# Performance work log

Hardware: AMD Instinct MI355X
Metric: run time of the kernel (lower is better)

## Reference

```python
import jax, jax.numpy as jnp
import numpy as np

B, S, HID = 1, 2048, 3584
NUM_HEADS, KV_HEADS, HEAD_DIM = 28, 4, 128
MROPE = [16, 24, 24]
HEAVY_RATIO, RECENT_RATIO, SINK, MIN_SEQ = 0.1, 0.1, 4, 1024
SCALING = HEAD_DIM ** -0.5
ROPE_THETA = 1000000.0


def rotate_half(x):
    h = x.shape[-1] // 2
    return jnp.concatenate([-x[..., h:], x[..., :h]], axis=-1)


def apply_mrope(q, k, cos, sin, mrope_section):
    # cos/sin: [3, B, S, head_dim]; interleave sections from the 3 position axes
    sec = mrope_section * 2
    splits = list(np.cumsum(sec)[:-1])
    cos_m = jnp.concatenate([m[i % 3] for i, m in enumerate(jnp.split(cos, splits, axis=-1))], axis=-1)[:, None]  # [B,1,S,D]
    sin_m = jnp.concatenate([m[i % 3] for i, m in enumerate(jnp.split(sin, splits, axis=-1))], axis=-1)[:, None]
    q_emb = q * cos_m + rotate_half(q) * sin_m
    k_emb = k * cos_m + rotate_half(k) * sin_m
    return q_emb, k_emb


def h2o_keep_mask(attn_weights, kv_len):
    # attn_weights: [B, H, Q, KV] post-softmax; accumulated score per head/key
    scores = attn_weights.sum(axis=(0, 2))  # [H, KV]
    heavy = max(1, int(HEAVY_RATIO * kv_len))
    recent = max(1, int(RECENT_RATIO * kv_len))
    keep = jnp.zeros((NUM_HEADS, kv_len), dtype=bool)
    ips = max(SINK * 2, int(0.2 * kv_len))  # image-protect prefix
    if kv_len > 3 * ips:
        keep = keep.at[:, :ips].set(True)
        ms = ips
    else:
        keep = keep.at[:, :SINK].set(True)
        ms = SINK
    keep = keep.at[:, kv_len - recent:].set(True)
    me = kv_len - recent
    k = min(heavy, me - ms)
    _, idx = jax.lax.top_k(scores[:, ms:me], k)  # [H, k]
    keep = keep.at[jnp.arange(NUM_HEADS)[:, None], idx + ms].set(True)
    return keep[None, :, None, :]  # [1, H, 1, KV]


def setup_inputs() -> dict:
    key = jax.random.key(0)
    ks = jax.random.split(key, 8)
    hidden_states = jax.random.normal(ks[0], (B, S, HID), jnp.float32)
    # additive causal mask
    causal = jnp.triu(jnp.full((S, S), -1e9, jnp.float32), k=1)
    attention_mask = causal[None, None]
    # mrope cos/sin (same positions on all 3 axes for text-only prefill)
    inv_freq = 1.0 / (ROPE_THETA ** (jnp.arange(0, HEAD_DIM, 2, dtype=jnp.float32) / HEAD_DIM))
    pos = jnp.arange(S, dtype=jnp.float32)
    freqs = pos[:, None] * inv_freq[None, :]            # [S, D/2]
    emb = jnp.concatenate([freqs, freqs], axis=-1)      # [S, D]
    cos = jnp.broadcast_to(jnp.cos(emb)[None, None], (3, B, S, HEAD_DIM))
    sin = jnp.broadcast_to(jnp.sin(emb)[None, None], (3, B, S, HEAD_DIM))
    sd = 0.02
    q_w = jax.random.normal(ks[1], (NUM_HEADS * HEAD_DIM, HID), jnp.float32) * sd
    q_b = jax.random.normal(ks[2], (NUM_HEADS * HEAD_DIM,), jnp.float32) * sd
    k_w = jax.random.normal(ks[3], (KV_HEADS * HEAD_DIM, HID), jnp.float32) * sd
    k_b = jax.random.normal(ks[4], (KV_HEADS * HEAD_DIM,), jnp.float32) * sd
    v_w = jax.random.normal(ks[5], (KV_HEADS * HEAD_DIM, HID), jnp.float32) * sd
    v_b = jax.random.normal(ks[6], (KV_HEADS * HEAD_DIM,), jnp.float32) * sd
    o_w = jax.random.normal(ks[7], (HID, NUM_HEADS * HEAD_DIM), jnp.float32) * sd
    return {"hidden_states": hidden_states, "attention_mask": attention_mask, "cos": cos, "sin": sin,
            "q_w": q_w, "q_b": q_b, "k_w": k_w, "k_b": k_b, "v_w": v_w, "v_b": v_b, "o_w": o_w}


def reference(hidden_states, attention_mask, cos, sin, q_w, q_b, k_w, k_b, v_w, v_b, o_w):
    b, s, _ = hidden_states.shape
    q = (hidden_states @ q_w.T + q_b).reshape(b, s, NUM_HEADS, HEAD_DIM).transpose(0, 2, 1, 3)
    k = (hidden_states @ k_w.T + k_b).reshape(b, s, KV_HEADS, HEAD_DIM).transpose(0, 2, 1, 3)
    v = (hidden_states @ v_w.T + v_b).reshape(b, s, KV_HEADS, HEAD_DIM).transpose(0, 2, 1, 3)
    q, k = apply_mrope(q, k, cos, sin, MROPE)
    n_rep = NUM_HEADS // KV_HEADS
    k = jnp.repeat(k, n_rep, axis=1)  # matches torch repeat_kv layout
    v = jnp.repeat(v, n_rep, axis=1)
    aw = jnp.einsum('bhqd,bhkd->bhqk', q, k) * SCALING + attention_mask
    aw = jax.nn.softmax(aw.astype(jnp.float32), axis=-1).astype(q.dtype)
    kv_len = s
    heavy = max(1, int(HEAVY_RATIO * kv_len))
    recent = max(1, int(RECENT_RATIO * kv_len))
    if kv_len >= MIN_SEQ and kv_len > SINK + recent + heavy:
        mask = h2o_keep_mask(jax.lax.stop_gradient(aw), kv_len)
        aw = aw * mask.astype(aw.dtype)
        aw = aw / jnp.clip(aw.sum(-1, keepdims=True), 1e-9)
    out = jnp.einsum('bhqk,bhkd->bhqd', aw, v)
    out = out.transpose(0, 2, 1, 3).reshape(b, s, NUM_HEADS * HEAD_DIM)
    return out @ o_w.T
```

## Files before the change

### kernel.cpp

```cpp
#include <hip/hip_runtime.h>
#include <hip/hip_bf16.h>
#include <stdint.h>

#define S_LEN 2048
#define HID 3584
#define NHEADS 28
#define KVHEADS 4
#define HD 128
#define QKV_N 4608
#define NREP 7
#define SCALE 0.08838834764831845f
#define NJOBS 896

typedef __attribute__((ext_vector_type(8))) short bf16x8;
typedef __attribute__((ext_vector_type(8))) _Float16 f16x8;
typedef __attribute__((ext_vector_type(4))) float f32x4;

#define MFMA_B16(a, b, c) __builtin_amdgcn_mfma_f32_16x16x32_bf16((a), (b), (c), 0, 0, 0)
#define MFMA_F16(a, b, c) __builtin_amdgcn_mfma_f32_16x16x32_f16((a), (b), (c), 0, 0, 0)

__device__ __forceinline__ void gl_lds16(const void* g, void* l) {
  __builtin_amdgcn_global_load_lds(
      (__attribute__((address_space(1))) void*)(void*)(g),
      (__attribute__((address_space(3))) void*)(l), 16, 0, 0);
}

__global__ void cvt_f32_f16(const float* __restrict__ src, _Float16* __restrict__ dst, int n4) {
  int i = blockIdx.x * 256 + threadIdx.x;
  if (i >= n4) return;
  float4 v = ((const float4*)src)[i];
  _Float16 t[4] = {(_Float16)v.x, (_Float16)v.y, (_Float16)v.z, (_Float16)v.w};
  ((uint2*)dst)[i] = *(const uint2*)t;
}

template <bool HAS_BIAS>
__global__ __launch_bounds__(256, 4) void gemm_f16(
    const _Float16* __restrict__ A, int lda,
    const _Float16* __restrict__ B, int ldb,
    const float* __restrict__ bias, float* __restrict__ C, int ldc, int K) {
  __shared__ _Float16 lA[128 * 64], lB[128 * 64];
  const int tid = threadIdx.x;
  const int lane = tid & 63;
  const int wid = tid >> 6;
  const int wr = wid >> 1, wc = wid & 1;
  const int l15 = lane & 15, l4 = lane >> 4;
  const int bm = blockIdx.y * 128, bn = blockIdx.x * 128;
  f32x4 acc[4][4] = {};
  for (int k0 = 0; k0 < K; k0 += 64) {
    __syncthreads();
#pragma unroll
    for (int it = 0; it < 4; ++it) {
      int c = it * 256 + tid;
      int rw = c >> 3, sl = c & 7;
      int gcol = (sl ^ (rw & 7)) << 3;
      int lo = (it * 256 + (tid & 192)) * 8;
      gl_lds16(A + (size_t)(bm + rw) * lda + (k0 + gcol), &lA[lo]);
      gl_lds16(B + (size_t)(bn + rw) * ldb + (k0 + gcol), &lB[lo]);
    }
    __syncthreads();
#pragma unroll
    for (int kk = 0; kk < 2; ++kk) {
      f16x8 af[4], bf[4];
#pragma unroll
      for (int m = 0; m < 4; ++m) {
        int rA = wr * 64 + m * 16 + l15;
        af[m] = *(const f16x8*)&lA[rA * 64 + (((kk * 4 + l4) ^ (rA & 7)) << 3)];
      }
#pragma unroll
      for (int n = 0; n < 4; ++n) {
        int rB = wc * 64 + n * 16 + l15;
        bf[n] = *(const f16x8*)&lB[rB * 64 + (((kk * 4 + l4) ^ (rB & 7)) << 3)];
      }
#pragma unroll
      for (int m = 0; m < 4; ++m)
#pragma unroll
        for (int n = 0; n < 4; ++n)
          acc[m][n] = MFMA_F16(af[m], bf[n], acc[m][n]);
    }
  }
#pragma unroll
  for (int m = 0; m < 4; ++m)
#pragma unroll
    for (int n = 0; n < 4; ++n)
#pragma unroll
      for (int r = 0; r < 4; ++r) {
        size_t row = bm + wr * 64 + m * 16 + l4 * 4 + r;
        size_t col = bn + wc * 64 + n * 16 + l15;
        float v = acc[m][n][r];
        if (HAS_BIAS) v += bias[col];
        C[row * ldc + col] = v;
      }
}

__global__ void rope_f16(const float* __restrict__ qf, const float* __restrict__ cb,
                         const float* __restrict__ sb,
                         _Float16* __restrict__ q16, _Float16* __restrict__ k16) {
  int idx = blockIdx.x * 256 + threadIdx.x;
  int d1 = idx & 63;
  int hh = (idx >> 6) & 31;
  int s = idx >> 11;
  if (s >= S_LEN) return;
  const float* row = qf + (size_t)s * QKV_N + (hh < NHEADS ? hh * HD : HID + (hh - NHEADS) * HD);
  int d2 = d1 + 64;
  int ax1 = (d1 < 32) ? 0 : 1;
  int ax2 = (d2 < 80) ? 1 : 2;
  float c1 = cb[(size_t)ax1 * S_LEN * HD + (size_t)s * HD + d1];
  float s1 = sb[(size_t)ax1 * S_LEN * HD + (size_t)s * HD + d1];
  float c2 = cb[(size_t)ax2 * S_LEN * HD + (size_t)s * HD + d2];
  float s2 = sb[(size_t)ax2 * S_LEN * HD + (size_t)s * HD + d2];
  float x1 = row[d1], x2 = row[d2];
  float y1 = x1 * c1 - x2 * s1;
  float y2 = x2 * c2 + x1 * s2;
  _Float16* dp;
  size_t base;
  if (hh < NHEADS) { dp = q16; base = (size_t)s * HID + hh * HD; }
  else { dp = k16; base = (size_t)s * 512 + (hh - NHEADS) * HD; }
  dp[base + d1] = (_Float16)y1;
  dp[base + d2] = (_Float16)y2;
}

__global__ void vtrans(const float* __restrict__ qf, __hip_bfloat16* __restrict__ vt) {
  __shared__ __hip_bfloat16 t[64][65];
  const int j = blockIdx.z;
  const int d0 = blockIdx.y * 64;
  const int k0 = blockIdx.x * 64;
  const int tid = threadIdx.x;
#pragma unroll
  for (int half = 0; half < 2; ++half) {
    int r = half * 32 + (tid >> 3);
    int c = (tid & 7) * 8;
    const float* p = qf + (size_t)(k0 + r) * QKV_N + (HID + 512) + j * HD + d0 + c;
    float4 a = ((const float4*)p)[0];
    float4 b = ((const float4*)p)[1];
    t[c + 0][r] = __float2bfloat16(a.x); t[c + 1][r] = __float2bfloat16(a.y);
    t[c + 2][r] = __float2bfloat16(a.z); t[c + 3][r] = __float2bfloat16(a.w);
    t[c + 4][r] = __float2bfloat16(b.x); t[c + 5][r] = __float2bfloat16(b.y);
    t[c + 6][r] = __float2bfloat16(b.z); t[c + 7][r] = __float2bfloat16(b.w);
  }
  __syncthreads();
#pragma unroll
  for (int half = 0; half < 2; ++half) {
    int r = half * 32 + (tid >> 3);
    int c = (tid & 7) * 8;
    __hip_bfloat16 tmp[8];
#pragma unroll
    for (int u = 0; u < 8; ++u) tmp[u] = t[r][c + u];
    *(bf16x8*)&vt[(size_t)j * (HD * S_LEN) + (size_t)(d0 + r) * S_LEN + k0 + c] = *(const bf16x8*)tmp;
  }
}

template <typename T>
__device__ __forceinline__ void stageK_sw(T* dst, const T* gsrc, int ldg, int tid) {
#pragma unroll
  for (int it = 0; it < 4; ++it) {
    int c = it * 256 + tid;
    int rw = c >> 4, sl = c & 15;
    int gcol = (sl ^ (rw & 7)) << 3;
    gl_lds16(gsrc + (size_t)rw * ldg + gcol, dst + (size_t)(it * 256 + (tid & 192)) * 8);
  }
}
__device__ __forceinline__ void stageV_sw(__hip_bfloat16* dst, const __hip_bfloat16* gsrc,
                                          int ldg, int tid) {
#pragma unroll
  for (int it = 0; it < 4; ++it) {
    int c = it * 256 + tid;
    int rw = c >> 3, sl = c & 7;
    int gcol = (sl ^ (rw & 7)) << 3;
    gl_lds16(gsrc + (size_t)rw * ldg + gcol, dst + (size_t)(it * 256 + (tid & 192)) * 8);
  }
}

__global__ __launch_bounds__(256, 2) void attn_ls(
    const _Float16* __restrict__ q16, const _Float16* __restrict__ k16,
    float* __restrict__ scores, int* __restrict__ ctr) {
  __shared__ _Float16 Kh[2][64 * 128];
  __shared__ int sj;
  const int tid = threadIdx.x;
  const int lane = tid & 63, w = tid >> 6;
  const int l15 = lane & 15, l4 = lane >> 4;
  const int sw = l15 & 7;
  for (;;) {
    __syncthreads();
    if (tid == 0) sj = atomicAdd(ctr, 1);
    __syncthreads();
    const int j = sj;
    if (j >= NJOBS) return;
    const int qb = 31 - j / 28, h = j % 28;
    const int hkv = h / NREP;
    const int nt = qb + 1;
    f16x8 qh[4];
    {
      const _Float16* qp = q16 + (size_t)(qb * 64 + w * 16 + l15) * HID + h * HD + l4 * 8;
#pragma unroll
      for (int kk = 0; kk < 4; ++kk) qh[kk] = *(const f16x8*)(qp + kk * 32);
    }
    float lsum[4] = {0.f, 0.f, 0.f, 0.f};
    stageK_sw(Kh[0], k16 + hkv * HD, 512, tid);
    __syncthreads();
    for (int kt = 0; kt < nt; ++kt) {
      if (kt + 1 < nt)
        stageK_sw(Kh[(kt + 1) & 1], k16 + (size_t)((kt + 1) * 64) * 512 + hkv * HD, 512, tid);
      const _Float16* Kc = Kh[kt & 1];
      f32x4 acc[4] = {};
#pragma unroll
      for (int kk = 0; kk < 4; ++kk)
#pragma unroll
        for (int n = 0; n < 4; ++n) {
          f16x8 bh = *(const f16x8*)&Kc[(n * 16 + l15) * 128 + (((kk * 4 + l4) ^ sw) << 3)];
          acc[n] = MFMA_F16(qh[kk], bh, acc[n]);
        }
      const bool diag = (kt == qb);
#pragma unroll
      for (int r = 0; r < 4; ++r) {
        int rowg = qb * 64 + w * 16 + l4 * 4 + r;
#pragma unroll
        for (int n = 0; n < 4; ++n)
          if (!(diag && (kt * 64 + n * 16 + l15) > rowg))
            lsum[r] += __expf(acc[n][r] * SCALE);
      }
      __syncthreads();
    }
    float invl[4];
#pragma unroll
    for (int r = 0; r < 4; ++r) {
      float s = lsum[r];
      s += __shfl_xor(s, 1);
      s += __shfl_xor(s, 2);
      s += __shfl_xor(s, 4);
      s += __shfl_xor(s, 8);
      invl[r] = 1.0f / s;
    }
    stageK_sw(Kh[0], k16 + hkv * HD, 512, tid);
    __syncthreads();
    for (int kt = 0; kt < nt; ++kt) {
      if (kt + 1 < nt)
        stageK_sw(Kh[(kt + 1) & 1], k16 + (size_t)((kt + 1) * 64) * 512 + hkv * HD, 512, tid);
      const _Float16* Kc = Kh[kt & 1];
      f32x4 acc[4] = {};
#pragma unroll
      for (int kk = 0; kk < 4; ++kk)
#pragma unroll
        for (int n = 0; n < 4; ++n) {
          f16x8 bh = *(const f16x8*)&Kc[(n * 16 + l15) * 128 + (((kk * 4 + l4) ^ sw) << 3)];
          acc[n] = MFMA_F16(qh[kk], bh, acc[n]);
        }
      const bool diag = (kt == qb);
      float colsum[4] = {0.f, 0.f, 0.f, 0.f};
#pragma unroll
      for (int r = 0; r < 4; ++r) {
        int rowg = qb * 64 + w * 16 + l4 * 4 + r;
#pragma unroll
        for (int n = 0; n < 4; ++n)
          if (!(diag && (kt * 64 + n * 16 + l15) > rowg))
            colsum[n] += __expf(acc[n][r] * SCALE) * invl[r];
      }
#pragma unroll
      for (int n = 0; n < 4; ++n) {
        colsum[n] += __shfl_xor(colsum[n], 16);
        colsum[n] += __shfl_xor(colsum[n], 32);
      }
      if (lane < 16) {
#pragma unroll
        for (int n = 0; n < 4; ++n)
          atomicAdd(&scores[h * S_LEN + kt * 64 + n * 16 + lane], colsum[n]);
      }
      __syncthreads();
    }
  }
}

__global__ void h2o_topk(const float* __restrict__ scores, unsigned char* __restrict__ keep) {
  const int h = blockIdx.x;
  const int tid = threadIdx.x;
  const int MS = 409, ME = 1844, REGN = 1435, KSEL = 204;
  __shared__ float sv[1435];
  __shared__ int cnt, eqn;
  __shared__ int eqlist[256];
  for (int i = tid; i < REGN; i += 256) sv[i] = scores[h * S_LEN + MS + i];
  for (int i = tid; i < S_LEN; i += 256)
    keep[h * S_LEN + i] = (i < MS || i >= ME) ? 1 : 0;
  __syncthreads();
  unsigned lo = 0u, hi = 0x7f800000u;
  while (hi - lo > 1u) {
    unsigned mid = lo + ((hi - lo) >> 1);
    if (tid == 0) cnt = 0;
    __syncthreads();
    int lc = 0;
    for (int i = tid; i < REGN; i += 256) lc += (__float_as_uint(sv[i]) >= mid) ? 1 : 0;
    if (lc) atomicAdd(&cnt, lc);
    __syncthreads();
    int c = cnt;
    __syncthreads();
    if (c >= KSEL) lo = mid;
    else hi = mid;
  }
  if (tid == 0) { cnt = 0; eqn = 0; }
  __syncthreads();
  int lgt = 0;
  for (int i = tid; i < REGN; i += 256) {
    unsigned b = __float_as_uint(sv[i]);
    if (b > lo) { keep[h * S_LEN + MS + i] = 1; lgt++; }
    else if (b == lo) {
      int p = atomicAdd(&eqn, 1);
      if (p < 256) eqlist[p] = i;
    }
  }
  if (lgt) atomicAdd(&cnt, lgt);
  __syncthreads();
  if (tid == 0) {
    int r = KSEL - cnt;
    int ne = eqn > 256 ? 256 : eqn;
    for (int t = 0; t < r; ++t) {
      int best = 0x7fffffff, bj = -1;
      for (int j = 0; j < ne; ++j)
        if (eqlist[j] < best) { best = eqlist[j]; bj = j; }
      if (bj < 0) break;
      keep[h * S_LEN + MS + best] = 1;
      eqlist[bj] = 0x7fffffff;
    }
  }
}

__global__ __launch_bounds__(256, 2) void attn_out(
    const _Float16* __restrict__ q16, const _Float16* __restrict__ k16,
    const __hip_bfloat16* __restrict__ vt, const unsigned char* __restrict__ keep,
    _Float16* __restrict__ ctx, int* __restrict__ ctr) {
  __shared__ _Float16 Kh[2][64 * 128];
  __shared__ __hip_bfloat16 Vtl[2][128 * 64];
  __shared__ __hip_bfloat16 Wt[4][16 * 64];
  __shared__ int sj;
  const int tid = threadIdx.x;
  const int lane = tid & 63, w = tid >> 6;
  const int l15 = lane & 15, l4 = lane >> 4;
  const int sw = l15 & 7;
  for (;;) {
    __syncthreads();
    if (tid == 0) sj = atomicAdd(ctr, 1);
    __syncthreads();
    const int j = sj;
    if (j >= NJOBS) return;
    const int qb = 31 - j / 28, h = j % 28;
    const int hkv = h / NREP;
    const int nt = qb + 1;
    f16x8 qh[4];
    {
      const _Float16* qp = q16 + (size_t)(qb * 64 + w * 16 + l15) * HID + h * HD + l4 * 8;
#pragma unroll
      for (int kk = 0; kk < 4; ++kk) qh[kk] = *(const f16x8*)(qp + kk * 32);
    }
    f32x4 o[8] = {};
    float dens[4] = {0.f, 0.f, 0.f, 0.f};
    stageK_sw(Kh[0], k16 + hkv * HD, 512, tid);
    stageV_sw(Vtl[0], vt + (size_t)hkv * (HD * S_LEN), S_LEN, tid);
    __syncthreads();
    for (int kt = 0; kt < nt; ++kt) {
      if (kt + 1 < nt) {
        stageK_sw(Kh[(kt + 1) & 1], k16 + (size_t)((kt + 1) * 64) * 512 + hkv * HD, 512, tid);
        stageV_sw(Vtl[(kt + 1) & 1], vt + (size_t)hkv * (HD * S_LEN) + (kt + 1) * 64, S_LEN, tid);
      }
      const _Float16* Kc = Kh[kt & 1];
      const __hip_bfloat16* Vc = Vtl[kt & 1];
      f32x4 acc[4] = {};
#pragma unroll
      for (int kk = 0; kk < 4; ++kk)
#pragma unroll
        for (int n = 0; n < 4; ++n) {
          f16x8 bh = *(const f16x8*)&Kc[(n * 16 + l15) * 128 + (((kk * 4 + l4) ^ sw) << 3)];
          acc[n] = MFMA_F16(qh[kk], bh, acc[n]);
        }
      const bool diag = (kt == qb);
      float kf[4];
#pragma unroll
      for (int n = 0; n < 4; ++n)
        kf[n] = (float)keep[h * S_LEN + kt * 64 + n * 16 + l15];
#pragma unroll
      for (int r = 0; r < 4; ++r) {
        int rowg = qb * 64 + w * 16 + l4 * 4 + r;
        int row16 = l4 * 4 + r;
#pragma unroll
        for (int n = 0; n < 4; ++n) {
          int coll = n * 16 + l15;
          float wv = 0.f;
          if (!diag || (kt * 64 + coll) <= rowg)
            wv = kf[n] * __expf(acc[n][r] * SCALE);
          dens[r] += wv;
          Wt[w][row16 * 64 + (coll ^ ((row16 & 7) << 3))] = __float2bfloat16(wv);
        }
      }
#pragma unroll
      for (int kk = 0; kk < 2; ++kk) {
        bf16x8 af = *(const bf16x8*)&Wt[w][l15 * 64 + ((kk * 32 + l4 * 8) ^ (sw << 3))];
#pragma unroll
        for (int n = 0; n < 8; ++n) {
          bf16x8 bf = *(const bf16x8*)&Vc[(n * 16 + l15) * 64 + (((kk * 4 + l4) ^ sw) << 3)];
          o[n] = MFMA_B16(af, bf, o[n]);
        }
      }
      __syncthreads();
    }
    float invd[4];
#pragma unroll
    for (int r = 0; r < 4; ++r) {
      float d = dens[r];
      d += __shfl_xor(d, 1);
      d += __shfl_xor(d, 2);
      d += __shfl_xor(d, 4);
      d += __shfl_xor(d, 8);
      invd[r] = 1.0f / fmaxf(d, 1e-30f);
    }
#pragma unroll
    for (int n = 0; n < 8; ++n)
#pragma unroll
      for (int r = 0; r < 4; ++r) {
        size_t row = qb * 64 + w * 16 + l4 * 4 + r;
        size_t col = h * HD + n * 16 + l15;
        ctx[row * HID + col] = (_Float16)(o[n][r] * invd[r]);
      }
  }
}

extern "C" void kernel_launch(void* const* d_in, const int* in_sizes, int n_in,
                              void* d_out, int out_size, void* d_ws, size_t ws_size,
                              hipStream_t stream) {
  const float* hidden = (const float*)d_in[0];
  const float* cosb = (const float*)d_in[2];
  const float* sinb = (const float*)d_in[3];
  const float* q_w = (const float*)d_in[4];
  const float* q_b = (const float*)d_in[5];
  const float* k_w = (const float*)d_in[6];
  const float* k_b = (const float*)d_in[7];
  const float* v_w = (const float*)d_in[8];
  const float* v_b = (const float*)d_in[9];
  const float* o_w = (const float*)d_in[10];

  char* ws = (char*)d_ws;
  float* qkv_f32 = (float*)(ws + 0);
  _Float16* hf16 = (_Float16*)(ws + 37748736);
  _Float16* wqkv16 = (_Float16*)(ws + 52428800);
  float* biasb = (float*)(ws + 85458944);
  _Float16* q16 = (_Float16*)(ws + 37748736);
  _Float16* wo16 = (_Float16*)(ws + 52428800);
  _Float16* k16 = (_Float16*)(ws + 85477376);
  __hip_bfloat16* vt = (__hip_bfloat16*)(ws + 87574528);
  float* scores = (float*)(ws + 89671680);
  unsigned char* keep = (unsigned char*)(ws + 89901056);
  int* ctrs = (int*)(ws + 89958400);
  _Float16* ctx16 = (_Float16*)(ws + 0);

  hipMemcpyAsync(biasb, q_b, 3584 * 4, hipMemcpyDeviceToDevice, stream);
  hipMemcpyAsync(biasb + 3584, k_b, 512 * 4, hipMemcpyDeviceToDevice, stream);
  hipMemcpyAsync(biasb + 4096, v_b, 512 * 4, hipMemcpyDeviceToDevice, stream);

  cvt_f32_f16<<<7168, 256, 0, stream>>>(hidden, hf16, 1835008);
  cvt_f32_f16<<<12544, 256, 0, stream>>>(q_w, wqkv16, 3211264);
  cvt_f32_f16<<<1792, 256, 0, stream>>>(k_w, wqkv16 + (size_t)3584 * 3584, 458752);
  cvt_f32_f16<<<1792, 256, 0, stream>>>(v_w, wqkv16 + (size_t)4096 * 3584, 458752);

  gemm_f16<true><<<dim3(36, 16), 256, 0, stream>>>(hf16, HID, wqkv16, HID,
                                                   biasb, qkv_f32, QKV_N, HID);

  cvt_f32_f16<<<12544, 256, 0, stream>>>(o_w, wo16, 3211264);

  rope_f16<<<16384, 256, 0, stream>>>(qkv_f32, cosb, sinb, q16, k16);
  vtrans<<<dim3(32, 2, 4), 256, 0, stream>>>(qkv_f32, vt);
  hipMemsetAsync(scores, 0, NHEADS * S_LEN * 4, stream);
  hipMemsetAsync(ctrs, 0, 8, stream);

  attn_ls<<<512, 256, 0, stream>>>(q16, k16, scores, &ctrs[0]);
  h2o_topk<<<28, 256, 0, stream>>>(scores, keep);
  attn_out<<<512, 256, 0, stream>>>(q16, k16, vt, keep, ctx16, &ctrs[1]);

  gemm_f16<false><<<dim3(28, 16), 256, 0, stream>>>(ctx16, HID, wo16, HID,
                                                    nullptr, (float*)d_out, HID, HID);
}
```

Measured before the change: 436.4 us.

## Double-buffer GEMM LDS tiles and raise attention score kernel occupancy

```diff
diff --git a/kernel.cpp b/kernel.cpp
--- a/kernel.cpp
+++ b/kernel.cpp
@@ -34,42 +34,52 @@
 }
 
 template <bool HAS_BIAS>
-__global__ __launch_bounds__(256, 4) void gemm_f16(
+__global__ __launch_bounds__(256, 2) void gemm_f16(
     const _Float16* __restrict__ A, int lda,
     const _Float16* __restrict__ B, int ldb,
     const float* __restrict__ bias, float* __restrict__ C, int ldc, int K) {
-  __shared__ _Float16 lA[128 * 64], lB[128 * 64];
+  __shared__ _Float16 lA[2][128 * 64], lB[2][128 * 64];
   const int tid = threadIdx.x;
   const int lane = tid & 63;
   const int wid = tid >> 6;
   const int wr = wid >> 1, wc = wid & 1;
   const int l15 = lane & 15, l4 = lane >> 4;
   const int bm = blockIdx.y * 128, bn = blockIdx.x * 128;
+  const int NK = K >> 6;
   f32x4 acc[4][4] = {};
-  for (int k0 = 0; k0 < K; k0 += 64) {
-    __syncthreads();
-#pragma unroll
-    for (int it = 0; it < 4; ++it) {
-      int c = it * 256 + tid;
-      int rw = c >> 3, sl = c & 7;
-      int gcol = (sl ^ (rw & 7)) << 3;
-      int lo = (it * 256 + (tid & 192)) * 8;
-      gl_lds16(A + (size_t)(bm + rw) * lda + (k0 + gcol), &lA[lo]);
-      gl_lds16(B + (size_t)(bn + rw) * ldb + (k0 + gcol), &lB[lo]);
-    }
-    __syncthreads();
+
+#define GEMM_STAGE(buf, k0)                                                      \
+  {                                                                              \
+    _Float16* dA = lA[buf];                                                      \
+    _Float16* dB = lB[buf];                                                      \
+    _Pragma("unroll") for (int it = 0; it < 4; ++it) {                           \
+      int c = it * 256 + tid;                                                    \
+      int rw = c >> 3, sl = c & 7;                                               \
+      int gcol = (sl ^ (rw & 7)) << 3;                                           \
+      int lo = (it * 256 + (tid & 192)) * 8;                                     \
+      gl_lds16(A + (size_t)(bm + rw) * lda + ((k0) + gcol), &dA[lo]);            \
+      gl_lds16(B + (size_t)(bn + rw) * ldb + ((k0) + gcol), &dB[lo]);            \
+    }                                                                            \
+  }
+
+  GEMM_STAGE(0, 0);
+  __syncthreads();
+  for (int ks = 0; ks < NK; ++ks) {
+    if (ks + 1 < NK) GEMM_STAGE((ks + 1) & 1, (ks + 1) * 64);
+    const _Float16* cA = lA[ks & 1];
+    const _Float16* cB = lB[ks & 1];
 #pragma unroll
     for (int kk = 0; kk < 2; ++kk) {
       f16x8 af[4], bf[4];
 #pragma unroll
       for (int m = 0; m < 4; ++m) {
         int rA = wr * 64 + m * 16 + l15;
-        af[m] = *(const f16x8*)&lA[rA * 64 + (((kk * 4 + l4) ^ (rA & 7)) << 3)];
+        af[m] = *(const f16x8*)&cA[rA * 64 + (((kk * 4 + l4) ^ (rA & 7)) << 3)];
       }
 #pragma unroll
       for (int n = 0; n < 4; ++n) {
         int rB = wc * 64 + n * 16 + l15;
-        bf[n] = *(const f16x8*)&lB[rB * 64 + (((kk * 4 + l4) ^ (rB & 7)) << 3)];
+        bf[n] = *(const f16x8*)&cB[rB * 64 + (((kk * 4 + l4) ^ (rB & 7)) << 3)];
       }
 #pragma unroll
       for (int m = 0; m < 4; ++m)
@@ -77,7 +87,9 @@
         for (int n = 0; n < 4; ++n)
           acc[m][n] = MFMA_F16(af[m], bf[n], acc[m][n]);
     }
-  }
+    __syncthreads();
+  }
+#undef GEMM_STAGE
 #pragma unroll
   for (int m = 0; m < 4; ++m)
 #pragma unroll
@@ -170,7 +182,7 @@
   }
 }
 
-__global__ __launch_bounds__(256, 2) void attn_ls(
+__global__ __launch_bounds__(256, 4) void attn_ls(
     const _Float16* __restrict__ q16, const _Float16* __restrict__ k16,
     float* __restrict__ scores, int* __restrict__ ctr) {
   __shared__ _Float16 Kh[2][64 * 128];
@@ -466,7 +478,7 @@
   hipMemsetAsync(scores, 0, NHEADS * S_LEN * 4, stream);
   hipMemsetAsync(ctrs, 0, 8, stream);
 
-  attn_ls<<<512, 256, 0, stream>>>(q16, k16, scores, &ctrs[0]);
+  attn_ls<<<1024, 256, 0, stream>>>(q16, k16, scores, &ctrs[0]);
   h2o_topk<<<28, 256, 0, stream>>>(scores, keep);
   attn_out<<<512, 256, 0, stream>>>(q16, k16, vt, keep, ctx16, &ctrs[1]);
 
```

After: 478.2 us. +9.6%, slower.
